# Kernel optimization log

Hardware: AMD Instinct MI355X
Metric: run time of the kernel (lower is better)

The kernel has to match this reference:

```python
import jax, jax.numpy as jnp
import numpy as np


def setup_inputs() -> dict:
    key = jax.random.key(0)
    x = jax.random.normal(key, (512, 2048, 7, 7), dtype=jnp.float32)
    return {"input": x, "dim": 2}


def reference(input, dim):
    # reshape to (B, 2048, 49), take mean of top-4 per row, output (B, 2048, 1, 1)
    feature = input.reshape(-1, 2048, 49)
    top4, _ = jax.lax.top_k(feature, 4)            # (B, 2048, 4)
    pooled = jnp.sum(top4, axis=2) / 4.0           # (B, 2048)
    return pooled[:, :, None, None]                # (B, 2048, 1, 1)
```

## Files before the change

kernel.cpp:

```cpp
#include <hip/hip_runtime.h>


#define ROW_LEN 49
#define ROWS_PER_BLOCK 256
#define BLOCK_THREADS 256
#define FLOATS_PER_BLOCK (ROWS_PER_BLOCK * ROW_LEN)
#define VEC4_PER_BLOCK (FLOATS_PER_BLOCK / 4)

__global__ __launch_bounds__(BLOCK_THREADS)
void apool_52286931861675_kernel(const float* __restrict__ x,
                                 float* __restrict__ out) {
    __shared__ float lds[FLOATS_PER_BLOCK];

    const float4* __restrict__ src =
        (const float4*)(x + (size_t)blockIdx.x * FLOATS_PER_BLOCK);
    float4* dst = (float4*)lds;
    #pragma unroll
    for (int i = 0; i < 13; ++i) {
        int idx = (int)threadIdx.x + i * BLOCK_THREADS;
        if (idx < VEC4_PER_BLOCK) dst[idx] = src[idx];
    }
    __syncthreads();

    const float* row = lds + (size_t)threadIdx.x * ROW_LEN;
    float m0 = -__builtin_inff();
    float m1 = m0, m2 = m0, m3 = m0;
    #pragma unroll
    for (int i = 0; i < ROW_LEN; ++i) {
        float v  = row[i];
        float t0 = fminf(m0, v);  m0 = fmaxf(m0, v);
        float t1 = fminf(m1, t0); m1 = fmaxf(m1, t0);
        float t2 = fminf(m2, t1); m2 = fmaxf(m2, t1);
        m3 = fmaxf(m3, t2);
    }

    out[(size_t)blockIdx.x * ROWS_PER_BLOCK + threadIdx.x] =
        (m0 + m1 + m2 + m3) * 0.25f;
}

extern "C" void kernel_launch(void* const* d_in, const int* in_sizes, int n_in,
                              void* d_out, int out_size, void* d_ws, size_t ws_size,
                              hipStream_t stream) {
    const float* x = (const float*)d_in[0];
    float* out = (float*)d_out;

    const int rows = out_size;
    const int grid = rows / ROWS_PER_BLOCK;

    apool_52286931861675_kernel<<<grid, BLOCK_THREADS, 0, stream>>>(x, out);
}
```

Baseline: 276.7 us.

## Split each row's top-4 across four lanes with shuffle merge, smaller blocks

Each block now handles 64 rows instead of 256, and four threads share one row, each scanning about 12 elements and then merging their partial top-4 lists with xor shuffles. This shrinks the per-block LDS footprint (about 12.5KB instead of 49KB), which allows more resident blocks (launch bounds hint of 8) and gives more latency hiding for the memory-bound load. Each thread's serial compare chain also gets shorter. In exchange it adds shuffle-merge work and runs four times as many blocks.

```diff
diff --git a/kernel.cpp b/kernel.cpp
--- a/kernel.cpp
+++ b/kernel.cpp
@@ -1,13 +1,22 @@
 #include <hip/hip_runtime.h>
+#include <float.h>
 
 
 #define ROW_LEN 49
-#define ROWS_PER_BLOCK 256
+#define ROWS_PER_BLOCK 64
 #define BLOCK_THREADS 256
 #define FLOATS_PER_BLOCK (ROWS_PER_BLOCK * ROW_LEN)
 #define VEC4_PER_BLOCK (FLOATS_PER_BLOCK / 4)
 
-__global__ __launch_bounds__(BLOCK_THREADS)
+__device__ __forceinline__ void top4_insert(float v, float& m0, float& m1,
+                                            float& m2, float& m3) {
+    float t0 = fminf(m0, v);  m0 = fmaxf(m0, v);
+    float t1 = fminf(m1, t0); m1 = fmaxf(m1, t0);
+    float t2 = fminf(m2, t1); m2 = fmaxf(m2, t1);
+    m3 = fmaxf(m3, t2);
+}
+
+__global__ __launch_bounds__(BLOCK_THREADS, 8)
 void apool_52286931861675_kernel(const float* __restrict__ x,
                                  float* __restrict__ out) {
     __shared__ float lds[FLOATS_PER_BLOCK];
@@ -16,26 +25,42 @@
         (const float4*)(x + (size_t)blockIdx.x * FLOATS_PER_BLOCK);
     float4* dst = (float4*)lds;
     #pragma unroll
-    for (int i = 0; i < 13; ++i) {
+    for (int i = 0; i < 4; ++i) {
         int idx = (int)threadIdx.x + i * BLOCK_THREADS;
         if (idx < VEC4_PER_BLOCK) dst[idx] = src[idx];
     }
     __syncthreads();
 
-    const float* row = lds + (size_t)threadIdx.x * ROW_LEN;
-    float m0 = -__builtin_inff();
-    float m1 = m0, m2 = m0, m3 = m0;
+    const int r = threadIdx.x >> 2;
+    const int q = threadIdx.x & 3;
+    const int start = (q == 0) ? 0 : (1 + 12 * q);
+    const int cnt   = (q == 0) ? 13 : 12;
+    const float* row = lds + r * ROW_LEN;
+
+    const float NEG = -FLT_MAX;
+    float m0 = NEG, m1 = NEG, m2 = NEG, m3 = NEG;
     #pragma unroll
-    for (int i = 0; i < ROW_LEN; ++i) {
-        float v  = row[i];
-        float t0 = fminf(m0, v);  m0 = fmaxf(m0, v);
-        float t1 = fminf(m1, t0); m1 = fmaxf(m1, t0);
-        float t2 = fminf(m2, t1); m2 = fmaxf(m2, t1);
-        m3 = fmaxf(m3, t2);
+    for (int i = 0; i < 13; ++i) {
+        float v = (i < cnt) ? row[start + i] : NEG;
+        top4_insert(v, m0, m1, m2, m3);
     }
 
-    out[(size_t)blockIdx.x * ROWS_PER_BLOCK + threadIdx.x] =
-        (m0 + m1 + m2 + m3) * 0.25f;
+    #pragma unroll
+    for (int k = 1; k <= 2; k <<= 1) {
+        float p0 = __shfl_xor(m0, k);
+        float p1 = __shfl_xor(m1, k);
+        float p2 = __shfl_xor(m2, k);
+        float p3 = __shfl_xor(m3, k);
+        top4_insert(p0, m0, m1, m2, m3);
+        top4_insert(p1, m0, m1, m2, m3);
+        top4_insert(p2, m0, m1, m2, m3);
+        top4_insert(p3, m0, m1, m2, m3);
+    }
+
+    if (q == 0) {
+        out[(size_t)blockIdx.x * ROWS_PER_BLOCK + r] =
+            (m0 + m1 + m2 + m3) * 0.25f;
+    }
 }
 
 extern "C" void kernel_launch(void* const* d_in, const int* in_sizes, int n_in,
```

Measured after the change: 276.3 us. About the same (-0.2%).
